# Kernel optimization log

Hardware: AMD Instinct MI355X
Metric: run time of the kernel (lower is better)

The kernel has to match this reference:

```python
import jax, jax.numpy as jnp
import numpy as np

B_SZ, SEQ, H, P, N, LBLK = 16, 2048, 16, 64, 16, 64  # batch, seqlen, heads, d_head, d_state, block_len


def setup_inputs() -> dict:
    key = jax.random.key(0)
    k1, k2, k3, k4 = jax.random.split(key, 4)
    X = jax.random.normal(k1, (B_SZ, SEQ, H, P), jnp.float32)
    # A is a per-step log-decay; real Mamba2 has A < 0 so exp(segsum) stays bounded
    A = -0.1 * jax.random.uniform(k2, (B_SZ, SEQ, H), jnp.float32)
    B = jax.random.normal(k3, (B_SZ, SEQ, H, N), jnp.float32)
    C = jax.random.normal(k4, (B_SZ, SEQ, H, N), jnp.float32)
    return {"X": X, "A": A, "B": B, "C": C}


def _exp_segsum(x):
    """x: (..., t). Returns exp(cumsum[i]-cumsum[j]) for j<=i, 0 above diagonal."""
    t = x.shape[-1]
    cs = jnp.cumsum(x, axis=-1)
    diff = cs[..., :, None] - cs[..., None, :]
    mask = jnp.tril(jnp.ones((t, t), dtype=bool))
    return jnp.where(mask, jnp.exp(jnp.where(mask, diff, 0.0)), 0.0)


def ssd_forward(X, A, B, C):
    b, s, h, p = X.shape
    n = B.shape[-1]
    c = s // LBLK
    # chunk: (b, c, l, h, *)
    Xb = X.reshape(b, c, LBLK, h, p)
    Bb = B.reshape(b, c, LBLK, h, n)
    Cb = C.reshape(b, c, LBLK, h, n)
    Ab = jnp.transpose(A.reshape(b, c, LBLK, h), (0, 3, 1, 2))  # (b, h, c, l)
    A_cs = jnp.cumsum(Ab, axis=-1)                               # (b, h, c, l)

    # 1. intra-chunk (diagonal block) output: kernel 1
    L = _exp_segsum(Ab)                                          # (b, h, c, l, s)
    CB = jnp.einsum("bclhn,bcshn->bhcls", Cb, Bb)               # (b, h, c, l, s)
    Y_diag = jnp.einsum("bhcls,bcshp->bclhp", CB * L, Xb)

    # 2. per-chunk end states: kernel 2
    decay_states = jnp.exp(A_cs[..., -1:] - A_cs)                # (b, h, c, l)
    states = jnp.einsum("bclhn,bhcl,bclhp->bchpn", Bb, decay_states, Xb)

    # 3. inter-chunk recurrence (zero initial state): kernel 3
    states = jnp.concatenate([jnp.zeros_like(states[:, :1]), states], axis=1)  # (b, c+1, h, p, n)
    A_last_pad = jnp.pad(A_cs[..., -1], ((0, 0), (0, 0), (1, 0)))              # (b, h, c+1)
    decay_chunk = _exp_segsum(A_last_pad)                                       # (b, h, c+1, c+1)
    new_states = jnp.einsum("bhzc,bchpn->bzhpn", decay_chunk, states)
    states_in = new_states[:, :-1]                                              # (b, c, h, p, n)

    # 4. off-diagonal (state -> output) contribution: kernel 4
    Y_off = jnp.einsum("bclhn,bchpn,bhcl->bclhp", Cb, states_in, jnp.exp(A_cs))

    return (Y_diag + Y_off).reshape(b, s, h, p)


def reference(X, A, B, C):
    return ssd_forward(X, A, B, C)
```

## Files before the change

### kernel.cpp

```cpp
#include <hip/hip_runtime.h>

#define BS 16
#define SEQL 2048
#define NH 16
#define PD 64
#define ND 16
#define LB 64
#define NC 32
#define NHP (NH * PD)
#define NHN (NH * ND)

typedef __attribute__((ext_vector_type(8))) short bf16x8;
typedef __attribute__((ext_vector_type(4))) float f32x4;

static __device__ __forceinline__ unsigned short f2bf(float x) {
  unsigned int u = __float_as_uint(x);
  return (unsigned short)((u + 0x7FFFu + ((u >> 16) & 1u)) >> 16);
}
static __device__ __forceinline__ unsigned int pk2(float a, float b) {
  return (unsigned int)f2bf(a) | ((unsigned int)f2bf(b) << 16);
}
static __device__ __forceinline__ void barrier_lgkm() {
  asm volatile("s_waitcnt lgkmcnt(0)" ::: "memory");
  __builtin_amdgcn_s_barrier();
  asm volatile("" ::: "memory");
}

__global__ __launch_bounds__(512) void ssd_fused(
    const float* __restrict__ Xg, const float* __restrict__ Ag,
    const float* __restrict__ Bg, const float* __restrict__ Cg,
    float* __restrict__ Yg) {
  const int h = blockIdx.x & (NH - 1);
  const int b = blockIdx.x >> 4;
  const int t = threadIdx.x;
  const int w = t >> 6;
  const int lane = t & 63;
  const int g = lane >> 4;
  const int cc = lane & 15;

  __shared__ __align__(16) unsigned short sXt[2][PD][64];
  __shared__ __align__(16) unsigned short sM[LB][LB + 8];
  __shared__ __align__(16) unsigned short sB[LB][ND + 8];
  __shared__ __align__(16) unsigned short sC[LB][ND + 8];
  __shared__ __align__(16) unsigned short sBdT[ND][LB + 8];
  __shared__ __align__(16) float sSTf[2][PD][ND + 4];
  __shared__ __align__(16) unsigned short sSTb[2][PD][ND + 8];

  const int xp0 = (t & 15) * 4, xl0 = (t >> 4) * 2;
  const int bl = t >> 3, bn0 = (t & 7) * 2;
  const int n_bt = t >> 5, l_bt = (t & 31) * 2;

  const int lb1 = (int)((0x33222110u >> (4 * w)) & 0xFu);
  const int sb1 = (int)((0x20210100u >> (4 * w)) & 0xFu);

  float4 px0, px1;
  float2 pb2, pc2;
  float pbA_v, pbB_v, pa;
  float er, rr, etot, er_n, rr_n, etot_n;

#define PREF(ci) do { \
    const size_t s0_ = (size_t)(b * SEQL + (ci) * LB); \
    px0 = *(const float4*)&Xg[(s0_ + xl0) * NHP + h * PD + xp0]; \
    px1 = *(const float4*)&Xg[(s0_ + xl0 + 1) * NHP + h * PD + xp0]; \
    pb2 = *(const float2*)&Bg[(s0_ + bl) * NHN + h * ND + bn0]; \
    pc2 = *(const float2*)&Cg[(s0_ + bl) * NHN + h * ND + bn0]; \
    pbA_v = Bg[(s0_ + l_bt) * NHN + h * ND + n_bt]; \
    pbB_v = Bg[(s0_ + l_bt + 1) * NHN + h * ND + n_bt]; \
    pa = Ag[(s0_ + lane) * NH + h]; \
  } while (0)

#define CUMSUM_STAGE(bufi) do { \
    float v_ = pa; \
    _Pragma("unroll") \
    for (int d_ = 1; d_ < 64; d_ <<= 1) { \
      float o_ = __shfl_up(v_, d_, 64); \
      if (lane >= d_) v_ += o_; \
    } \
    er_n = expf(v_); rr_n = expf(-v_); etot_n = __shfl(er_n, 63); \
    _Pragma("unroll") \
    for (int j_ = 0; j_ < 4; ++j_) { \
      const int p_ = xp0 + j_; \
      const int idx_ = (((xl0 >> 3) ^ ((p_ >> 3) & 7)) << 3) | (xl0 & 7); \
      *(unsigned int*)&sXt[bufi][p_][idx_] = pk2((&px0.x)[j_], (&px1.x)[j_]); \
    } \
    { const float el_ = __shfl(er_n, bl); \
      *(unsigned int*)&sB[bl][bn0] = pk2(pb2.x, pb2.y); \
      *(unsigned int*)&sC[bl][bn0] = pk2(el_ * pc2.x, el_ * pc2.y); } \
    { const float d0_ = etot_n * __shfl(rr_n, l_bt); \
      const float d1_ = etot_n * __shfl(rr_n, l_bt + 1); \
      *(unsigned int*)&sBdT[n_bt][l_bt] = pk2(d0_ * pbA_v, d1_ * pbB_v); } \
  } while (0)

  const bf16x8 zf8 = {0, 0, 0, 0, 0, 0, 0, 0};

  auto xfrag = [&](int buf, int p_, int l0_) -> bf16x8 {
    const int idx_ = (((l0_ >> 3) ^ ((p_ >> 3) & 7)) << 3);
    return *(const bf16x8*)&sXt[buf][p_][idx_];
  };

  auto p1tile = [&](int lb_, int sb_) {
    const int l_ = lb_ * 16 + cc;
    bf16x8 cf = zf8, bfr = zf8;
    if (g < 2) {
      cf = *(const bf16x8*)&sC[l_][g * 8];
      bfr = *(const bf16x8*)&sB[sb_ * 16 + cc][g * 8];
    }
    f32x4 z4 = {0.f, 0.f, 0.f, 0.f};
    f32x4 d = __builtin_amdgcn_mfma_f32_16x16x32_bf16(bfr, cf, z4, 0, 0, 0);
    float mm[4];
#pragma unroll
    for (int r = 0; r < 4; ++r) {
      const int srow = sb_ * 16 + 4 * g + r;
      mm[r] = d[r] * __shfl(rr, srow);
      if (sb_ == lb_ && (4 * g + r) > cc) mm[r] = 0.f;
    }
    uint2 o;
    o.x = pk2(mm[0], mm[1]);
    o.y = pk2(mm[2], mm[3]);
    *(uint2*)&sM[l_][sb_ * 16 + g * 4] = o;
  };

  for (int i = t; i < PD * (ND + 4); i += 512) ((float*)sSTf[0])[i] = 0.f;
  for (int i = t; i < PD * (ND + 8); i += 512) ((unsigned short*)sSTb[0])[i] = 0;
  PREF(0);
  CUMSUM_STAGE(0);
  er = er_n; rr = rr_n; etot = etot_n;
  PREF(1);
  barrier_lgkm();

  const int lbY = w & 3;
  const int pbb = (w < 4) ? 0 : 2;
  const int pS = (w - 4) * 16 + cc;

  for (int c = 0; c < NC; ++c) {
    const int cur = c & 1, nxt = cur ^ 1;

    p1tile(lb1, sb1);
    if (w >= 6) p1tile(lb1, sb1 + 1);
    if (w == 4) *(uint2*)&sM[cc][16 + g * 4] = make_uint2(0u, 0u);
    if (w == 5) *(uint2*)&sM[32 + cc][48 + g * 4] = make_uint2(0u, 0u);

    bf16x8 cfY = zf8;
    if (g < 2) cfY = *(const bf16x8*)&sC[lbY * 16 + cc][g * 8];
    bf16x8 stf[2], xfa[2], xfb[2];
#pragma unroll
    for (int pbi = 0; pbi < 2; ++pbi) {
      const int p_ = (pbb + pbi) * 16 + cc;
      stf[pbi] = zf8;
      if (g < 2) stf[pbi] = *(const bf16x8*)&sSTb[cur][p_][g * 8];
      xfa[pbi] = xfrag(cur, p_, g * 8);
      xfb[pbi] = zf8;
      if (lbY >= 2) xfb[pbi] = xfrag(cur, p_, 32 + g * 8);
    }
    bf16x8 ad0 = zf8, ad1 = zf8, xt0 = zf8, xt1 = zf8;
    float4 stold = make_float4(0.f, 0.f, 0.f, 0.f);
    if (w >= 4) {
      ad0 = *(const bf16x8*)&sBdT[cc][g * 8];
      ad1 = *(const bf16x8*)&sBdT[cc][32 + g * 8];
      xt0 = xfrag(cur, pS, g * 8);
      xt1 = xfrag(cur, pS, 32 + g * 8);
      stold = *(const float4*)&sSTf[cur][pS][4 * g];
    }

    barrier_lgkm();

    {
      const int lY = lbY * 16 + cc;
      bf16x8 a0 = *(const bf16x8*)&sM[lY][g * 8];
      bf16x8 a1 = zf8;
      if (lbY >= 2) a1 = *(const bf16x8*)&sM[lY][32 + g * 8];
#pragma unroll
      for (int pbi = 0; pbi < 2; ++pbi) {
        const int p_ = (pbb + pbi) * 16 + cc;
        f32x4 acc = {0.f, 0.f, 0.f, 0.f};
        acc = __builtin_amdgcn_mfma_f32_16x16x32_bf16(cfY, stf[pbi], acc, 0, 0, 0);
        acc = __builtin_amdgcn_mfma_f32_16x16x32_bf16(a0, xfa[pbi], acc, 0, 0, 0);
        if (lbY >= 2)
          acc = __builtin_amdgcn_mfma_f32_16x16x32_bf16(a1, xfb[pbi], acc, 0, 0, 0);
        const size_t yb =
            ((size_t)(b * SEQL + c * LB + lbY * 16 + 4 * g)) * NHP + h * PD + p_;
#pragma unroll
        for (int r = 0; r < 4; ++r) Yg[yb + (size_t)r * NHP] = acc[r];
      }
    }
    if (w >= 4) {
      f32x4 s4 = {0.f, 0.f, 0.f, 0.f};
      s4 = __builtin_amdgcn_mfma_f32_16x16x32_bf16(ad0, xt0, s4, 0, 0, 0);
      s4 = __builtin_amdgcn_mfma_f32_16x16x32_bf16(ad1, xt1, s4, 0, 0, 0);
      float4 nw;
      nw.x = stold.x * etot + s4[0];
      nw.y = stold.y * etot + s4[1];
      nw.z = stold.z * etot + s4[2];
      nw.w = stold.w * etot + s4[3];
      *(float4*)&sSTf[nxt][pS][4 * g] = nw;
      uint2 ub;
      ub.x = pk2(nw.x, nw.y);
      ub.y = pk2(nw.z, nw.w);
      *(uint2*)&sSTb[nxt][pS][4 * g] = ub;
    }
    if (c + 1 < NC) {
      CUMSUM_STAGE(nxt);
      if (c + 2 < NC) PREF(c + 2);
      er = er_n; rr = rr_n; etot = etot_n;
    }

    barrier_lgkm();
  }
#undef PREF
#undef CUMSUM_STAGE
}

extern "C" void kernel_launch(void* const* d_in, const int* in_sizes, int n_in,
                              void* d_out, int out_size, void* d_ws, size_t ws_size,
                              hipStream_t stream) {
  (void)in_sizes; (void)n_in; (void)out_size; (void)d_ws; (void)ws_size;
  const float* X = (const float*)d_in[0];
  const float* A = (const float*)d_in[1];
  const float* B = (const float*)d_in[2];
  const float* C = (const float*)d_in[3];
  float* Y = (float*)d_out;
  ssd_fused<<<BS * NH, 512, 0, stream>>>(X, A, B, C, Y);
}
```

Measured before the change: 93.42 us.

## Split head dimension across two blocks of 256 threads each

The grid is doubled so that each (batch, head) pair is handled by two blocks, each covering half of the P dimension with 256 threads. This raises the block count from 256 to 512 to fill more CUs on the device. The cost is that the CB/decay matrix and the cumsum are recomputed in both blocks, and the B/C loads are duplicated. The pipeline also changes from a two-barrier double-buffered X layout to a single-buffer scheme with three __syncthreads per chunk, which reduces overlap.

```diff
diff --git a/kernel.cpp b/kernel.cpp
--- a/kernel.cpp
+++ b/kernel.cpp
@@ -9,6 +9,7 @@
 #define NC 32
 #define NHP (NH * PD)
 #define NHN (NH * ND)
+#define PH 32
 
 typedef __attribute__((ext_vector_type(8))) short bf16x8;
 typedef __attribute__((ext_vector_type(4))) float f32x4;
@@ -20,82 +21,55 @@
 static __device__ __forceinline__ unsigned int pk2(float a, float b) {
   return (unsigned int)f2bf(a) | ((unsigned int)f2bf(b) << 16);
 }
-static __device__ __forceinline__ void barrier_lgkm() {
-  asm volatile("s_waitcnt lgkmcnt(0)" ::: "memory");
-  __builtin_amdgcn_s_barrier();
-  asm volatile("" ::: "memory");
-}
-
-__global__ __launch_bounds__(512) void ssd_fused(
+
+__global__ __launch_bounds__(256) void ssd_fused(
     const float* __restrict__ Xg, const float* __restrict__ Ag,
     const float* __restrict__ Bg, const float* __restrict__ Cg,
     float* __restrict__ Yg) {
-  const int h = blockIdx.x & (NH - 1);
-  const int b = blockIdx.x >> 4;
+  const int bh = blockIdx.x & 255;
+  const int ph = blockIdx.x >> 8;
+  const int h = bh & (NH - 1);
+  const int b = bh >> 4;
+  const int pc0 = h * PD + ph * PH;
   const int t = threadIdx.x;
   const int w = t >> 6;
   const int lane = t & 63;
   const int g = lane >> 4;
   const int cc = lane & 15;
 
-  __shared__ __align__(16) unsigned short sXt[2][PD][64];
+  __shared__ __align__(16) unsigned short sXt[PH][64];
   __shared__ __align__(16) unsigned short sM[LB][LB + 8];
   __shared__ __align__(16) unsigned short sB[LB][ND + 8];
   __shared__ __align__(16) unsigned short sC[LB][ND + 8];
   __shared__ __align__(16) unsigned short sBdT[ND][LB + 8];
-  __shared__ __align__(16) float sSTf[2][PD][ND + 4];
-  __shared__ __align__(16) unsigned short sSTb[2][PD][ND + 8];
-
-  const int xp0 = (t & 15) * 4, xl0 = (t >> 4) * 2;
-  const int bl = t >> 3, bn0 = (t & 7) * 2;
-  const int n_bt = t >> 5, l_bt = (t & 31) * 2;
-
-  const int lb1 = (int)((0x33222110u >> (4 * w)) & 0xFu);
-  const int sb1 = (int)((0x20210100u >> (4 * w)) & 0xFu);
-
-  float4 px0, px1;
-  float2 pb2, pc2;
-  float pbA_v, pbB_v, pa;
-  float er, rr, etot, er_n, rr_n, etot_n;
+  __shared__ __align__(16) float sSTf[2][PH][ND + 4];
+  __shared__ __align__(16) unsigned short sSTb[2][PH][ND + 8];
+
+  const int xl0 = (t >> 3) * 2, xp0 = (t & 7) * 4;
+  const int bcr = t >> 2, bcq = (t & 3) * 4;
+  const int btn = t >> 4, btl = (t & 15) * 4;
+
+  float4 px0, px1, pb4, pc4;
+  float pa, pt0, pt1, pt2, pt3;
+  float er, rr, etot;
 
 #define PREF(ci) do { \
     const size_t s0_ = (size_t)(b * SEQL + (ci) * LB); \
-    px0 = *(const float4*)&Xg[(s0_ + xl0) * NHP + h * PD + xp0]; \
-    px1 = *(const float4*)&Xg[(s0_ + xl0 + 1) * NHP + h * PD + xp0]; \
-    pb2 = *(const float2*)&Bg[(s0_ + bl) * NHN + h * ND + bn0]; \
-    pc2 = *(const float2*)&Cg[(s0_ + bl) * NHN + h * ND + bn0]; \
-    pbA_v = Bg[(s0_ + l_bt) * NHN + h * ND + n_bt]; \
-    pbB_v = Bg[(s0_ + l_bt + 1) * NHN + h * ND + n_bt]; \
+    px0 = *(const float4*)&Xg[(s0_ + xl0) * NHP + pc0 + xp0]; \
+    px1 = *(const float4*)&Xg[(s0_ + xl0 + 1) * NHP + pc0 + xp0]; \
+    pb4 = *(const float4*)&Bg[(s0_ + bcr) * NHN + h * ND + bcq]; \
+    pc4 = *(const float4*)&Cg[(s0_ + bcr) * NHN + h * ND + bcq]; \
+    pt0 = Bg[(s0_ + btl) * NHN + h * ND + btn]; \
+    pt1 = Bg[(s0_ + btl + 1) * NHN + h * ND + btn]; \
+    pt2 = Bg[(s0_ + btl + 2) * NHN + h * ND + btn]; \
+    pt3 = Bg[(s0_ + btl + 3) * NHN + h * ND + btn]; \
     pa = Ag[(s0_ + lane) * NH + h]; \
   } while (0)
 
-#define CUMSUM_STAGE(bufi) do { \
-    float v_ = pa; \
-    _Pragma("unroll") \
-    for (int d_ = 1; d_ < 64; d_ <<= 1) { \
-      float o_ = __shfl_up(v_, d_, 64); \
-      if (lane >= d_) v_ += o_; \
-    } \
-    er_n = expf(v_); rr_n = expf(-v_); etot_n = __shfl(er_n, 63); \
-    _Pragma("unroll") \
-    for (int j_ = 0; j_ < 4; ++j_) { \
-      const int p_ = xp0 + j_; \
-      const int idx_ = (((xl0 >> 3) ^ ((p_ >> 3) & 7)) << 3) | (xl0 & 7); \
-      *(unsigned int*)&sXt[bufi][p_][idx_] = pk2((&px0.x)[j_], (&px1.x)[j_]); \
-    } \
-    { const float el_ = __shfl(er_n, bl); \
-      *(unsigned int*)&sB[bl][bn0] = pk2(pb2.x, pb2.y); \
-      *(unsigned int*)&sC[bl][bn0] = pk2(el_ * pc2.x, el_ * pc2.y); } \
-    { const float d0_ = etot_n * __shfl(rr_n, l_bt); \
-      const float d1_ = etot_n * __shfl(rr_n, l_bt + 1); \
-      *(unsigned int*)&sBdT[n_bt][l_bt] = pk2(d0_ * pbA_v, d1_ * pbB_v); } \
-  } while (0)
-
   const bf16x8 zf8 = {0, 0, 0, 0, 0, 0, 0, 0};
 
-  auto xfrag = [&](int buf, int p_, int l0_) -> bf16x8 {
-    const int idx_ = (((l0_ >> 3) ^ ((p_ >> 3) & 7)) << 3);
-    return *(const bf16x8*)&sXt[buf][p_][idx_];
+  auto xfrag = [&](int p_, int l0_) -> bf16x8 {
+    return *(const bf16x8*)&sXt[p_][((l0_ >> 3) ^ (p_ & 7)) << 3];
   };
 
   auto p1tile = [&](int lb_, int sb_) {
@@ -110,8 +84,7 @@
     float mm[4];
 #pragma unroll
     for (int r = 0; r < 4; ++r) {
-      const int srow = sb_ * 16 + 4 * g + r;
-      mm[r] = d[r] * __shfl(rr, srow);
+      mm[r] = d[r] * __shfl(rr, sb_ * 16 + 4 * g + r);
       if (sb_ == lb_ && (4 * g + r) > cc) mm[r] = 0.f;
     }
     uint2 o;
@@ -120,94 +93,114 @@
     *(uint2*)&sM[l_][sb_ * 16 + g * 4] = o;
   };
 
-  for (int i = t; i < PD * (ND + 4); i += 512) ((float*)sSTf[0])[i] = 0.f;
-  for (int i = t; i < PD * (ND + 8); i += 512) ((unsigned short*)sSTb[0])[i] = 0;
+  for (int i = t; i < PH * (ND + 4); i += 256) ((float*)sSTf[0])[i] = 0.f;
+  for (int i = t; i < PH * (ND + 8); i += 256) ((unsigned short*)sSTb[0])[i] = 0;
   PREF(0);
-  CUMSUM_STAGE(0);
-  er = er_n; rr = rr_n; etot = etot_n;
-  PREF(1);
-  barrier_lgkm();
-
-  const int lbY = w & 3;
-  const int pbb = (w < 4) ? 0 : 2;
-  const int pS = (w - 4) * 16 + cc;
 
   for (int c = 0; c < NC; ++c) {
     const int cur = c & 1, nxt = cur ^ 1;
 
-    p1tile(lb1, sb1);
-    if (w >= 6) p1tile(lb1, sb1 + 1);
-    if (w == 4) *(uint2*)&sM[cc][16 + g * 4] = make_uint2(0u, 0u);
-    if (w == 5) *(uint2*)&sM[32 + cc][48 + g * 4] = make_uint2(0u, 0u);
-
-    bf16x8 cfY = zf8;
-    if (g < 2) cfY = *(const bf16x8*)&sC[lbY * 16 + cc][g * 8];
-    bf16x8 stf[2], xfa[2], xfb[2];
-#pragma unroll
-    for (int pbi = 0; pbi < 2; ++pbi) {
-      const int p_ = (pbb + pbi) * 16 + cc;
-      stf[pbi] = zf8;
-      if (g < 2) stf[pbi] = *(const bf16x8*)&sSTb[cur][p_][g * 8];
-      xfa[pbi] = xfrag(cur, p_, g * 8);
-      xfb[pbi] = zf8;
-      if (lbY >= 2) xfb[pbi] = xfrag(cur, p_, 32 + g * 8);
-    }
-    bf16x8 ad0 = zf8, ad1 = zf8, xt0 = zf8, xt1 = zf8;
-    float4 stold = make_float4(0.f, 0.f, 0.f, 0.f);
-    if (w >= 4) {
-      ad0 = *(const bf16x8*)&sBdT[cc][g * 8];
-      ad1 = *(const bf16x8*)&sBdT[cc][32 + g * 8];
-      xt0 = xfrag(cur, pS, g * 8);
-      xt1 = xfrag(cur, pS, 32 + g * 8);
-      stold = *(const float4*)&sSTf[cur][pS][4 * g];
-    }
-
-    barrier_lgkm();
-
     {
-      const int lY = lbY * 16 + cc;
+      float v = pa;
+#pragma unroll
+      for (int d = 1; d < 64; d <<= 1) {
+        float o = __shfl_up(v, d, 64);
+        if (lane >= d) v += o;
+      }
+      er = expf(v);
+      rr = expf(-v);
+      etot = __shfl(er, 63);
+#pragma unroll
+      for (int j = 0; j < 4; ++j) {
+        const int p_ = xp0 + j;
+        const int idx = (((xl0 >> 3) ^ (p_ & 7)) << 3) | (xl0 & 7);
+        *(unsigned int*)&sXt[p_][idx] = pk2((&px0.x)[j], (&px1.x)[j]);
+      }
+      {
+        const float el_ = __shfl(er, bcr);
+        uint2 ub, uc;
+        ub.x = pk2(pb4.x, pb4.y);
+        ub.y = pk2(pb4.z, pb4.w);
+        uc.x = pk2(el_ * pc4.x, el_ * pc4.y);
+        uc.y = pk2(el_ * pc4.z, el_ * pc4.w);
+        *(uint2*)&sB[bcr][bcq] = ub;
+        *(uint2*)&sC[bcr][bcq] = uc;
+      }
+      {
+        const float d0 = etot * __shfl(rr, btl);
+        const float d1 = etot * __shfl(rr, btl + 1);
+        const float d2 = etot * __shfl(rr, btl + 2);
+        const float d3 = etot * __shfl(rr, btl + 3);
+        uint2 ut;
+        ut.x = pk2(d0 * pt0, d1 * pt1);
+        ut.y = pk2(d2 * pt2, d3 * pt3);
+        *(uint2*)&sBdT[btn][btl] = ut;
+      }
+    }
+    if (c + 1 < NC) PREF(c + 1);
+    __syncthreads();
+
+    {
+      const int lbA = (int)((0x0233u >> (4 * w)) & 0xFu);
+      const int sbA = (int)((0x0020u >> (4 * w)) & 0xFu);
+      const int lbB = (int)((0x1233u >> (4 * w)) & 0xFu);
+      const int sbB = (int)((0x0131u >> (4 * w)) & 0xFu);
+      p1tile(lbA, sbA);
+      p1tile(lbB, sbB);
+      if (w >= 2) {
+        const int k = (w == 2) ? 2 : 1;
+        p1tile(k, k);
+      }
+      if (w == 0) *(uint2*)&sM[cc][16 + g * 4] = make_uint2(0u, 0u);
+      if (w == 1) *(uint2*)&sM[32 + cc][48 + g * 4] = make_uint2(0u, 0u);
+    }
+    __syncthreads();
+
+    {
+      const int lY = w * 16 + cc;
+      bf16x8 cfY = zf8;
+      if (g < 2) cfY = *(const bf16x8*)&sC[lY][g * 8];
       bf16x8 a0 = *(const bf16x8*)&sM[lY][g * 8];
       bf16x8 a1 = zf8;
-      if (lbY >= 2) a1 = *(const bf16x8*)&sM[lY][32 + g * 8];
-#pragma unroll
-      for (int pbi = 0; pbi < 2; ++pbi) {
-        const int p_ = (pbb + pbi) * 16 + cc;
+      if (w >= 2) a1 = *(const bf16x8*)&sM[lY][32 + g * 8];
+#pragma unroll
+      for (int pb = 0; pb < 2; ++pb) {
+        const int p_ = pb * 16 + cc;
+        bf16x8 stf = zf8;
+        if (g < 2) stf = *(const bf16x8*)&sSTb[cur][p_][g * 8];
         f32x4 acc = {0.f, 0.f, 0.f, 0.f};
-        acc = __builtin_amdgcn_mfma_f32_16x16x32_bf16(cfY, stf[pbi], acc, 0, 0, 0);
-        acc = __builtin_amdgcn_mfma_f32_16x16x32_bf16(a0, xfa[pbi], acc, 0, 0, 0);
-        if (lbY >= 2)
-          acc = __builtin_amdgcn_mfma_f32_16x16x32_bf16(a1, xfb[pbi], acc, 0, 0, 0);
+        acc = __builtin_amdgcn_mfma_f32_16x16x32_bf16(cfY, stf, acc, 0, 0, 0);
+        acc = __builtin_amdgcn_mfma_f32_16x16x32_bf16(a0, xfrag(p_, g * 8), acc, 0, 0, 0);
+        if (w >= 2)
+          acc = __builtin_amdgcn_mfma_f32_16x16x32_bf16(a1, xfrag(p_, 32 + g * 8), acc, 0, 0, 0);
         const size_t yb =
-            ((size_t)(b * SEQL + c * LB + lbY * 16 + 4 * g)) * NHP + h * PD + p_;
+            ((size_t)(b * SEQL + c * LB + w * 16 + 4 * g)) * NHP + pc0 + p_;
 #pragma unroll
         for (int r = 0; r < 4; ++r) Yg[yb + (size_t)r * NHP] = acc[r];
       }
-    }
-    if (w >= 4) {
-      f32x4 s4 = {0.f, 0.f, 0.f, 0.f};
-      s4 = __builtin_amdgcn_mfma_f32_16x16x32_bf16(ad0, xt0, s4, 0, 0, 0);
-      s4 = __builtin_amdgcn_mfma_f32_16x16x32_bf16(ad1, xt1, s4, 0, 0, 0);
-      float4 nw;
-      nw.x = stold.x * etot + s4[0];
-      nw.y = stold.y * etot + s4[1];
-      nw.z = stold.z * etot + s4[2];
-      nw.w = stold.w * etot + s4[3];
-      *(float4*)&sSTf[nxt][pS][4 * g] = nw;
-      uint2 ub;
-      ub.x = pk2(nw.x, nw.y);
-      ub.y = pk2(nw.z, nw.w);
-      *(uint2*)&sSTb[nxt][pS][4 * g] = ub;
-    }
-    if (c + 1 < NC) {
-      CUMSUM_STAGE(nxt);
-      if (c + 2 < NC) PREF(c + 2);
-      er = er_n; rr = rr_n; etot = etot_n;
-    }
-
-    barrier_lgkm();
+      if (w < 2) {
+        const int pS = w * 16 + cc;
+        bf16x8 ad0 = *(const bf16x8*)&sBdT[cc][g * 8];
+        bf16x8 ad1 = *(const bf16x8*)&sBdT[cc][32 + g * 8];
+        f32x4 s4 = {0.f, 0.f, 0.f, 0.f};
+        s4 = __builtin_amdgcn_mfma_f32_16x16x32_bf16(ad0, xfrag(pS, g * 8), s4, 0, 0, 0);
+        s4 = __builtin_amdgcn_mfma_f32_16x16x32_bf16(ad1, xfrag(pS, 32 + g * 8), s4, 0, 0, 0);
+        float4 old = *(const float4*)&sSTf[cur][pS][4 * g];
+        float4 nw;
+        nw.x = old.x * etot + s4[0];
+        nw.y = old.y * etot + s4[1];
+        nw.z = old.z * etot + s4[2];
+        nw.w = old.w * etot + s4[3];
+        *(float4*)&sSTf[nxt][pS][4 * g] = nw;
+        uint2 ub;
+        ub.x = pk2(nw.x, nw.y);
+        ub.y = pk2(nw.z, nw.w);
+        *(uint2*)&sSTb[nxt][pS][4 * g] = ub;
+      }
+    }
+    __syncthreads();
   }
 #undef PREF
-#undef CUMSUM_STAGE
 }
 
 extern "C" void kernel_launch(void* const* d_in, const int* in_sizes, int n_in,
@@ -219,5 +212,5 @@
   const float* B = (const float*)d_in[2];
   const float* C = (const float*)d_in[3];
   float* Y = (float*)d_out;
-  ssd_fused<<<BS * NH, 512, 0, stream>>>(X, A, B, C, Y);
-}
+  ssd_fused<<<2 * BS * NH, 256, 0, stream>>>(X, A, B, C, Y);
+}
```

Result: slower. 123.9 us (+32.6%).

## Restructure chunk loop: double-buffer B/C/Bd, split waves into output vs state roles

Applied to the files above, without the earlier changes.

Replaces the software-pipelined schedule with a simpler per-chunk flow. All 8 waves build the masked CB tile into sM, then waves 0-3 compute all four p-blocks of Y while waves 4-7 update the chunk state. The B, C and decayed-B staging buffers are double-buffered, and the global prefetch is now issued only one chunk ahead, after the mask stage. The old prefetch-two-ahead pipelining and the balanced work split are lost. Y waves now carry twice the MFMA work while state waves carry little, so the load imbalance and shorter prefetch distance could expose latency.

```diff
diff --git a/kernel.cpp b/kernel.cpp
--- a/kernel.cpp
+++ b/kernel.cpp
@@ -20,11 +20,6 @@
 static __device__ __forceinline__ unsigned int pk2(float a, float b) {
   return (unsigned int)f2bf(a) | ((unsigned int)f2bf(b) << 16);
 }
-static __device__ __forceinline__ void barrier_lgkm() {
-  asm volatile("s_waitcnt lgkmcnt(0)" ::: "memory");
-  __builtin_amdgcn_s_barrier();
-  asm volatile("" ::: "memory");
-}
 
 __global__ __launch_bounds__(512) void ssd_fused(
     const float* __restrict__ Xg, const float* __restrict__ Ag,
@@ -40,23 +35,20 @@
 
   __shared__ __align__(16) unsigned short sXt[2][PD][64];
   __shared__ __align__(16) unsigned short sM[LB][LB + 8];
-  __shared__ __align__(16) unsigned short sB[LB][ND + 8];
-  __shared__ __align__(16) unsigned short sC[LB][ND + 8];
-  __shared__ __align__(16) unsigned short sBdT[ND][LB + 8];
+  __shared__ __align__(16) unsigned short sB[2][LB][ND + 8];
+  __shared__ __align__(16) unsigned short sC[2][LB][ND + 8];
+  __shared__ __align__(16) unsigned short sBdT[2][ND][LB + 8];
   __shared__ __align__(16) float sSTf[2][PD][ND + 4];
   __shared__ __align__(16) unsigned short sSTb[2][PD][ND + 8];
 
-  const int xp0 = (t & 15) * 4, xl0 = (t >> 4) * 2;
+  const int xl0 = (t >> 4) * 2, xp0 = (t & 15) * 4;
   const int bl = t >> 3, bn0 = (t & 7) * 2;
   const int n_bt = t >> 5, l_bt = (t & 31) * 2;
-
-  const int lb1 = (int)((0x33222110u >> (4 * w)) & 0xFu);
-  const int sb1 = (int)((0x20210100u >> (4 * w)) & 0xFu);
 
   float4 px0, px1;
   float2 pb2, pc2;
   float pbA_v, pbB_v, pa;
-  float er, rr, etot, er_n, rr_n, etot_n;
+  float er, rr, etot;
 
 #define PREF(ci) do { \
     const size_t s0_ = (size_t)(b * SEQL + (ci) * LB); \
@@ -76,135 +68,112 @@
       float o_ = __shfl_up(v_, d_, 64); \
       if (lane >= d_) v_ += o_; \
     } \
-    er_n = expf(v_); rr_n = expf(-v_); etot_n = __shfl(er_n, 63); \
+    er = expf(v_); rr = expf(-v_); etot = __shfl(er, 63); \
     _Pragma("unroll") \
     for (int j_ = 0; j_ < 4; ++j_) { \
       const int p_ = xp0 + j_; \
       const int idx_ = (((xl0 >> 3) ^ ((p_ >> 3) & 7)) << 3) | (xl0 & 7); \
       *(unsigned int*)&sXt[bufi][p_][idx_] = pk2((&px0.x)[j_], (&px1.x)[j_]); \
     } \
-    { const float el_ = __shfl(er_n, bl); \
-      *(unsigned int*)&sB[bl][bn0] = pk2(pb2.x, pb2.y); \
-      *(unsigned int*)&sC[bl][bn0] = pk2(el_ * pc2.x, el_ * pc2.y); } \
-    { const float d0_ = etot_n * __shfl(rr_n, l_bt); \
-      const float d1_ = etot_n * __shfl(rr_n, l_bt + 1); \
-      *(unsigned int*)&sBdT[n_bt][l_bt] = pk2(d0_ * pbA_v, d1_ * pbB_v); } \
+    { const float el_ = __shfl(er, bl); \
+      *(unsigned int*)&sB[bufi][bl][bn0] = pk2(pb2.x, pb2.y); \
+      *(unsigned int*)&sC[bufi][bl][bn0] = pk2(el_ * pc2.x, el_ * pc2.y); } \
+    { const float d0_ = etot * __shfl(rr, l_bt); \
+      const float d1_ = etot * __shfl(rr, l_bt + 1); \
+      *(unsigned int*)&sBdT[bufi][n_bt][l_bt] = pk2(d0_ * pbA_v, d1_ * pbB_v); } \
   } while (0)
 
   const bf16x8 zf8 = {0, 0, 0, 0, 0, 0, 0, 0};
 
   auto xfrag = [&](int buf, int p_, int l0_) -> bf16x8 {
-    const int idx_ = (((l0_ >> 3) ^ ((p_ >> 3) & 7)) << 3);
-    return *(const bf16x8*)&sXt[buf][p_][idx_];
-  };
-
-  auto p1tile = [&](int lb_, int sb_) {
-    const int l_ = lb_ * 16 + cc;
-    bf16x8 cf = zf8, bfr = zf8;
-    if (g < 2) {
-      cf = *(const bf16x8*)&sC[l_][g * 8];
-      bfr = *(const bf16x8*)&sB[sb_ * 16 + cc][g * 8];
-    }
-    f32x4 z4 = {0.f, 0.f, 0.f, 0.f};
-    f32x4 d = __builtin_amdgcn_mfma_f32_16x16x32_bf16(bfr, cf, z4, 0, 0, 0);
-    float mm[4];
-#pragma unroll
-    for (int r = 0; r < 4; ++r) {
-      const int srow = sb_ * 16 + 4 * g + r;
-      mm[r] = d[r] * __shfl(rr, srow);
-      if (sb_ == lb_ && (4 * g + r) > cc) mm[r] = 0.f;
-    }
-    uint2 o;
-    o.x = pk2(mm[0], mm[1]);
-    o.y = pk2(mm[2], mm[3]);
-    *(uint2*)&sM[l_][sb_ * 16 + g * 4] = o;
+    return *(const bf16x8*)&sXt[buf][p_][(((l0_ >> 3) ^ ((p_ >> 3) & 7)) << 3)];
   };
 
   for (int i = t; i < PD * (ND + 4); i += 512) ((float*)sSTf[0])[i] = 0.f;
   for (int i = t; i < PD * (ND + 8); i += 512) ((unsigned short*)sSTb[0])[i] = 0;
   PREF(0);
   CUMSUM_STAGE(0);
-  er = er_n; rr = rr_n; etot = etot_n;
-  PREF(1);
-  barrier_lgkm();
-
-  const int lbY = w & 3;
-  const int pbb = (w < 4) ? 0 : 2;
-  const int pS = (w - 4) * 16 + cc;
 
   for (int c = 0; c < NC; ++c) {
-    const int cur = c & 1, nxt = cur ^ 1;
+    const int db = c & 1, nb = db ^ 1;
 
-    p1tile(lb1, sb1);
-    if (w >= 6) p1tile(lb1, sb1 + 1);
-    if (w == 4) *(uint2*)&sM[cc][16 + g * 4] = make_uint2(0u, 0u);
-    if (w == 5) *(uint2*)&sM[32 + cc][48 + g * 4] = make_uint2(0u, 0u);
+    __syncthreads();
 
-    bf16x8 cfY = zf8;
-    if (g < 2) cfY = *(const bf16x8*)&sC[lbY * 16 + cc][g * 8];
-    bf16x8 stf[2], xfa[2], xfb[2];
+    {
+      const int lb1 = w & 3;
+      const int l = lb1 * 16 + cc;
+      bf16x8 cf = zf8;
+      if (g < 2) cf = *(const bf16x8*)&sC[db][l][g * 8];
 #pragma unroll
-    for (int pbi = 0; pbi < 2; ++pbi) {
-      const int p_ = (pbb + pbi) * 16 + cc;
-      stf[pbi] = zf8;
-      if (g < 2) stf[pbi] = *(const bf16x8*)&sSTb[cur][p_][g * 8];
-      xfa[pbi] = xfrag(cur, p_, g * 8);
-      xfb[pbi] = zf8;
-      if (lbY >= 2) xfb[pbi] = xfrag(cur, p_, 32 + g * 8);
-    }
-    bf16x8 ad0 = zf8, ad1 = zf8, xt0 = zf8, xt1 = zf8;
-    float4 stold = make_float4(0.f, 0.f, 0.f, 0.f);
-    if (w >= 4) {
-      ad0 = *(const bf16x8*)&sBdT[cc][g * 8];
-      ad1 = *(const bf16x8*)&sBdT[cc][32 + g * 8];
-      xt0 = xfrag(cur, pS, g * 8);
-      xt1 = xfrag(cur, pS, 32 + g * 8);
-      stold = *(const float4*)&sSTf[cur][pS][4 * g];
+      for (int ii = 0; ii < 2; ++ii) {
+        const int sb = (w < 4 ? 0 : 2) + ii;
+        uint2 out = make_uint2(0u, 0u);
+        if (sb <= lb1) {
+          bf16x8 bfr = zf8;
+          if (g < 2) bfr = *(const bf16x8*)&sB[db][sb * 16 + cc][g * 8];
+          f32x4 z4 = {0.f, 0.f, 0.f, 0.f};
+          f32x4 d = __builtin_amdgcn_mfma_f32_16x16x32_bf16(bfr, cf, z4, 0, 0, 0);
+          float m[4];
+#pragma unroll
+          for (int r = 0; r < 4; ++r) {
+            m[r] = d[r] * __shfl(rr, sb * 16 + 4 * g + r);
+            if (sb == lb1 && (4 * g + r) > cc) m[r] = 0.f;
+          }
+          out.x = pk2(m[0], m[1]);
+          out.y = pk2(m[2], m[3]);
+        }
+        *(uint2*)&sM[l][sb * 16 + g * 4] = out;
+      }
     }
 
-    barrier_lgkm();
+    __syncthreads();
 
-    {
-      const int lY = lbY * 16 + cc;
-      bf16x8 a0 = *(const bf16x8*)&sM[lY][g * 8];
+    if (c + 1 < NC) PREF(c + 1);
+
+    if (w < 4) {
+      const int lb = w;
+      const int l = lb * 16 + cc;
+      bf16x8 cf = zf8;
+      if (g < 2) cf = *(const bf16x8*)&sC[db][l][g * 8];
+      bf16x8 a0 = *(const bf16x8*)&sM[l][g * 8];
       bf16x8 a1 = zf8;
-      if (lbY >= 2) a1 = *(const bf16x8*)&sM[lY][32 + g * 8];
+      if (lb >= 2) a1 = *(const bf16x8*)&sM[l][32 + g * 8];
 #pragma unroll
-      for (int pbi = 0; pbi < 2; ++pbi) {
-        const int p_ = (pbb + pbi) * 16 + cc;
+      for (int pb = 0; pb < 4; ++pb) {
+        const int p = pb * 16 + cc;
+        bf16x8 stf = zf8;
+        if (g < 2) stf = *(const bf16x8*)&sSTb[db][p][g * 8];
         f32x4 acc = {0.f, 0.f, 0.f, 0.f};
-        acc = __builtin_amdgcn_mfma_f32_16x16x32_bf16(cfY, stf[pbi], acc, 0, 0, 0);
-        acc = __builtin_amdgcn_mfma_f32_16x16x32_bf16(a0, xfa[pbi], acc, 0, 0, 0);
-        if (lbY >= 2)
-          acc = __builtin_amdgcn_mfma_f32_16x16x32_bf16(a1, xfb[pbi], acc, 0, 0, 0);
+        acc = __builtin_amdgcn_mfma_f32_16x16x32_bf16(cf, stf, acc, 0, 0, 0);
+        acc = __builtin_amdgcn_mfma_f32_16x16x32_bf16(a0, xfrag(db, p, g * 8), acc, 0, 0, 0);
+        if (lb >= 2)
+          acc = __builtin_amdgcn_mfma_f32_16x16x32_bf16(a1, xfrag(db, p, 32 + g * 8), acc, 0, 0, 0);
         const size_t yb =
-            ((size_t)(b * SEQL + c * LB + lbY * 16 + 4 * g)) * NHP + h * PD + p_;
+            ((size_t)(b * SEQL + c * LB + lb * 16 + 4 * g)) * NHP + h * PD + p;
 #pragma unroll
         for (int r = 0; r < 4; ++r) Yg[yb + (size_t)r * NHP] = acc[r];
       }
-    }
-    if (w >= 4) {
+    } else {
+      const int pS = (w - 4) * 16 + cc;
+      bf16x8 ad0 = *(const bf16x8*)&sBdT[db][cc][g * 8];
+      bf16x8 ad1 = *(const bf16x8*)&sBdT[db][cc][32 + g * 8];
       f32x4 s4 = {0.f, 0.f, 0.f, 0.f};
-      s4 = __builtin_amdgcn_mfma_f32_16x16x32_bf16(ad0, xt0, s4, 0, 0, 0);
-      s4 = __builtin_amdgcn_mfma_f32_16x16x32_bf16(ad1, xt1, s4, 0, 0, 0);
+      s4 = __builtin_amdgcn_mfma_f32_16x16x32_bf16(ad0, xfrag(db, pS, g * 8), s4, 0, 0, 0);
+      s4 = __builtin_amdgcn_mfma_f32_16x16x32_bf16(ad1, xfrag(db, pS, 32 + g * 8), s4, 0, 0, 0);
+      float4 old = *(const float4*)&sSTf[db][pS][4 * g];
       float4 nw;
-      nw.x = stold.x * etot + s4[0];
-      nw.y = stold.y * etot + s4[1];
-      nw.z = stold.z * etot + s4[2];
-      nw.w = stold.w * etot + s4[3];
-      *(float4*)&sSTf[nxt][pS][4 * g] = nw;
+      nw.x = old.x * etot + s4[0];
+      nw.y = old.y * etot + s4[1];
+      nw.z = old.z * etot + s4[2];
+      nw.w = old.w * etot + s4[3];
+      *(float4*)&sSTf[nb][pS][4 * g] = nw;
       uint2 ub;
       ub.x = pk2(nw.x, nw.y);
       ub.y = pk2(nw.z, nw.w);
-      *(uint2*)&sSTb[nxt][pS][4 * g] = ub;
-    }
-    if (c + 1 < NC) {
-      CUMSUM_STAGE(nxt);
-      if (c + 2 < NC) PREF(c + 2);
-      er = er_n; rr = rr_n; etot = etot_n;
+      *(uint2*)&sSTb[nb][pS][4 * g] = ub;
     }
 
-    barrier_lgkm();
+    if (c + 1 < NC) CUMSUM_STAGE(nb);
   }
 #undef PREF
 #undef CUMSUM_STAGE
```

Result: slower. 107.1 us (+14.6%).
